# Optimization experiments

Hardware: AMD Instinct MI355X
Metric: run time of the kernel (lower is better)

## Reference

```python
import math
import jax, jax.numpy as jnp
import numpy as np

D_IN = 768      # input_hidden_dim
H = 512         # IDLU_hidden_dim
E = 64          # num_entity
B = 32          # batch_size (mentions)
P = 197         # num_patch (incl. CLS)
RHO = 4.0
EPS = 1e-5


def setup_inputs() -> dict:
    key = jax.random.key(0)
    ks = jax.random.split(key, 16)
    s = 1.0 / math.sqrt(D_IN)
    return {
        "entity_cls": jax.random.normal(ks[0], (E, D_IN), jnp.float32),
        "entity_tokens": jax.random.normal(ks[1], (E, P, D_IN), jnp.float32),
        "mention_image_cls": jax.random.normal(ks[2], (B, D_IN), jnp.float32),
        "mention_image_tokens": jax.random.normal(ks[3], (B, P, D_IN), jnp.float32),
        "mention_patch_mask": jax.random.uniform(ks[4], (B, P), jnp.float32),
        "Wq": jax.random.normal(ks[5], (D_IN, H), jnp.float32) * s,
        "bq": jnp.zeros((H,), jnp.float32),
        "Wk": jax.random.normal(ks[6], (D_IN, H), jnp.float32) * s,
        "bk": jnp.zeros((H,), jnp.float32),
        "Wv": jax.random.normal(ks[7], (D_IN, H), jnp.float32) * s,
        "bv": jnp.zeros((H,), jnp.float32),
        "Wcls": jax.random.normal(ks[8], (D_IN, H), jnp.float32) * s,
        "bcls": jnp.zeros((H,), jnp.float32),
        "ln_g": jnp.ones((H,), jnp.float32),
        "ln_b": jnp.zeros((H,), jnp.float32),
    }


def _layer_norm(x, g, b):
    mu = jnp.mean(x, axis=-1, keepdims=True)
    var = jnp.mean(jnp.square(x - mu), axis=-1, keepdims=True)
    return (x - mu) * jax.lax.rsqrt(var + EPS) * g + b


def reference(entity_cls, entity_tokens, mention_image_cls, mention_image_tokens,
              mention_patch_mask, Wq, bq, Wk, bk, Wv, bv, Wcls, bcls, ln_g, ln_b):
    entity_cls_fc = entity_cls @ Wcls + bcls                      # [E, H]
    q = entity_tokens @ Wq + bq                                   # [E, P, H]
    k = mention_image_tokens @ Wk + bk                            # [B, P, H]
    v = mention_image_tokens @ Wv + bv                            # [B, P, H]
    # broadcast entity x mention attention: [E, B, P, P]
    scores = jnp.einsum('eph,bqh->ebpq', q, k) / math.sqrt(H)
    # additive mask only on the first query row (CLS)
    scores = scores.at[:, :, 0, :].add(RHO * mention_patch_mask[None, :, :])
    probs = jax.nn.softmax(scores, axis=-1)                       # [E, B, P, P]
    context = jnp.einsum('ebpq,bqh->ebph', probs, v)              # [E, B, P, H]
    context = jnp.mean(context, axis=-2)                          # [E, B, H]
    context = _layer_norm(context, ln_g, ln_b)
    g2l = jnp.sum(entity_cls_fc[:, None, :] * context, axis=-1).T # [B, E]
    g2g = mention_image_cls @ entity_cls.T                        # [B, E]
    return (g2l + g2g) / 2
```

## Files before the change

kernel.cpp:

```cpp
#include <hip/hip_runtime.h>
#include <stdint.h>

#define EN 64
#define BN 32
#define PN 197
#define DIN 768
#define HH 512
#define RHO_ 4.0f

typedef __attribute__((ext_vector_type(8))) short bf16x8;
typedef __attribute__((ext_vector_type(4))) float f32x4;

__device__ __forceinline__ ushort f2bf(float f){
  unsigned u = __float_as_uint(f);
  u += 0x7FFFu + ((u >> 16) & 1u);
  return (ushort)(u >> 16);
}
__device__ __forceinline__ float bf2f(ushort h){ return __uint_as_float(((unsigned)h) << 16); }

#define GLOAD_LDS16(g, l) __builtin_amdgcn_global_load_lds( \
    (const __attribute__((address_space(1))) void*)(g), \
    (__attribute__((address_space(3))) void*)(l), 16, 0, 0)

__global__ __launch_bounds__(256) void prep_kernel(
    const float* __restrict__ etok, const float* __restrict__ mtok,
    const float* __restrict__ ecls, const float* __restrict__ bq,
    ushort* __restrict__ a_ent, ushort* __restrict__ a_men, ushort* __restrict__ a_cls,
    float* __restrict__ bq_s)
{
  int g = blockIdx.x*256 + threadIdx.x;
  int st = gridDim.x*256;
  const float s = 0.04419417382415922f;
  for (int i=g; i<(EN*PN*DIN)/4; i+=st){
    float4 v = ((const float4*)etok)[i];
    ushort4 o; o.x=f2bf(v.x); o.y=f2bf(v.y); o.z=f2bf(v.z); o.w=f2bf(v.w);
    ((ushort4*)a_ent)[i] = o;
  }
  for (int i=g; i<(BN*PN*DIN)/4; i+=st){
    float4 v = ((const float4*)mtok)[i];
    ushort4 o; o.x=f2bf(v.x); o.y=f2bf(v.y); o.z=f2bf(v.z); o.w=f2bf(v.w);
    ((ushort4*)a_men)[i] = o;
  }
  for (int i=g; i<(EN*DIN)/4; i+=st){
    float4 v = ((const float4*)ecls)[i];
    ushort4 o; o.x=f2bf(v.x); o.y=f2bf(v.y); o.z=f2bf(v.z); o.w=f2bf(v.w);
    ((ushort4*)a_cls)[i] = o;
  }
  for (int i=g; i<HH; i+=st) bq_s[i] = bq[i]*s;
}

__global__ __launch_bounds__(256) void w_transpose(
    const float* __restrict__ Wq, const float* __restrict__ Wk,
    const float* __restrict__ Wv, const float* __restrict__ Wc,
    ushort* __restrict__ Wt)
{
  __shared__ float tl[64][65];
  int mat = blockIdx.z;
  const float* src = (mat==0)?Wq:(mat==1)?Wk:(mat==2)?Wv:Wc;
  float sc = (mat==0)? 0.04419417382415922f : 1.0f;
  int k0 = blockIdx.x*64;
  int n0 = blockIdx.y*64;
  int tid = threadIdx.x;
  int c = tid & 63, r0 = tid >> 6;
  #pragma unroll
  for (int i=0;i<16;++i){
    int r = r0 + i*4;
    tl[r][c] = src[(size_t)(k0+r)*HH + n0+c];
  }
  __syncthreads();
  ushort* dst = Wt + (size_t)mat*HH*DIN;
  #pragma unroll
  for (int i=0;i<16;++i){
    int r = r0 + i*4;
    dst[(size_t)(n0+r)*DIN + k0+c] = f2bf(tl[c][r]*sc);
  }
}

__global__ __launch_bounds__(256) void gemm_proj(
    const ushort* __restrict__ a_ent, const ushort* __restrict__ a_men, const ushort* __restrict__ a_cls,
    const ushort* __restrict__ Wt,
    const float* __restrict__ bq_s, const float* __restrict__ bk,
    const float* __restrict__ bv, const float* __restrict__ bc,
    ushort* __restrict__ qo, ushort* __restrict__ ko, ushort* __restrict__ vo,
    float* __restrict__ co)
{
  int x = blockIdx.x;
  int op, mt;
  if (x < 99)        { op = 0; mt = x; }
  else if (x < 149)  { op = 1; mt = x - 99; }
  else if (x < 199)  { op = 2; mt = x - 149; }
  else               { op = 3; mt = 0; }
  int M = (op==0)? EN*PN : (op==3)? EN : BN*PN;
  int m0 = mt*128;
  const ushort* A  = (op==0)? a_ent : (op==3)? a_cls : a_men;
  const ushort* Bw = Wt + (size_t)op*HH*DIN;
  const float* bias = (op==0)? bq_s : (op==1)? bk : (op==2)? bv : bc;
  int n0 = blockIdx.y*128;
  int Mm1 = M-1;

  __shared__ ushort As[128*40];
  __shared__ ushort Bs[128*40];
  int tid = threadIdx.x;
  int lane = tid & 63, wid = tid >> 6;
  int l15 = lane & 15, lg = lane >> 4;
  int wm = wid >> 1, wn = wid & 1;

  f32x4 acc[16];
  #pragma unroll
  for (int i=0;i<16;++i){ f32x4 z = {0.f,0.f,0.f,0.f}; acc[i] = z; }

  bf16x8 sA[2], sB[2];
  #pragma unroll
  for (int i=0;i<2;++i){
    int u = tid + i*256; int row = u>>2; int ko8 = (u&3)*8;
    int rA = m0+row; rA = rA>Mm1 ? Mm1 : rA;
    sA[i] = *(const bf16x8*)(A  + (size_t)rA*DIN + ko8);
    sB[i] = *(const bf16x8*)(Bw + (size_t)(n0+row)*DIN + ko8);
  }
  for (int kt=0; kt<DIN/32; ++kt){
    #pragma unroll
    for (int i=0;i<2;++i){
      int u = tid + i*256; int row = u>>2; int ko8 = (u&3)*8;
      *(bf16x8*)(&As[row*40 + ko8]) = sA[i];
      *(bf16x8*)(&Bs[row*40 + ko8]) = sB[i];
    }
    __syncthreads();
    if (kt < DIN/32 - 1){
      int k0 = (kt+1)*32;
      #pragma unroll
      for (int i=0;i<2;++i){
        int u = tid + i*256; int row = u>>2; int ko8 = (u&3)*8;
        int rA = m0+row; rA = rA>Mm1 ? Mm1 : rA;
        sA[i] = *(const bf16x8*)(A  + (size_t)rA*DIN + k0 + ko8);
        sB[i] = *(const bf16x8*)(Bw + (size_t)(n0+row)*DIN + k0 + ko8);
      }
    }
    bf16x8 af[4], bfg[4];
    #pragma unroll
    for (int t=0;t<4;++t){
      af[t]  = *(const bf16x8*)(&As[(wm*64 + t*16 + l15)*40 + lg*8]);
      bfg[t] = *(const bf16x8*)(&Bs[(wn*64 + t*16 + l15)*40 + lg*8]);
    }
    #pragma unroll
    for (int am=0; am<4; ++am)
      #pragma unroll
      for (int bn=0; bn<4; ++bn)
        acc[am*4+bn] = __builtin_amdgcn_mfma_f32_16x16x32_bf16(af[am], bfg[bn], acc[am*4+bn], 0, 0, 0);
    __syncthreads();
  }

  #pragma unroll
  for (int bn=0; bn<4; ++bn){
    int col = n0 + wn*64 + bn*16 + l15;
    float bval = bias[col];
    #pragma unroll
    for (int am=0; am<4; ++am){
      #pragma unroll
      for (int r=0;r<4;++r){
        int row = m0 + wm*64 + am*16 + lg*4 + r;
        if (row < M){
          float v = acc[am*4+bn][r] + bval;
          if (op==3)      co[(size_t)row*HH + col] = v;
          else if (op==0) qo[(size_t)row*HH + col] = f2bf(v);
          else if (op==1) ko[(size_t)row*HH + col] = f2bf(v);
          else            vo[(size_t)row*HH + col] = f2bf(v);
        }
      }
    }
  }
}

__global__ __launch_bounds__(512) void attn_kernel(
    const ushort* __restrict__ qw, const ushort* __restrict__ kw, const ushort* __restrict__ vw,
    const float* __restrict__ cls_fc, const float* __restrict__ maskp,
    const float* __restrict__ mcls, const float* __restrict__ ecls,
    const float* __restrict__ lng, const float* __restrict__ lnb,
    float* __restrict__ outp)
{
  int bid = blockIdx.x;
  int b = bid >> 5;
  int e0 = (bid & 31) * 2;

  __shared__ ushort klds[2][1664*8];
  __shared__ float w_lds[2][208];
  __shared__ float red[32];

  int tid = threadIdx.x;
  int lane = tid & 63, wid = tid >> 6;
  int l15 = lane & 15, lg = (lane >> 4) & 3;

  for (int i=tid; i<416; i+=512) ((float*)w_lds)[i] = 0.f;

  const ushort* kb = kw + (size_t)b*PN*HH;
  const ushort* qb0 = qw + (size_t)e0*PN*HH;
  const ushort* qb1 = qw + (size_t)(e0+1)*PN*HH;

  auto issue = [&](int bf, int kc){
    #pragma unroll
    for (int i=0;i<4;++i){
      int L = tid + i*512;
      if (L < 1664){
        int col = L >> 3, j = L & 7;
        int cg = col > 196 ? 196 : col;
        const ushort* src = kb + (size_t)cg*HH + kc*64 + ((j ^ (col & 7)) * 8);
        ushort* dst = &klds[bf][ (wid*64 + i*512) * 8 ];
        GLOAD_LDS16(src, dst);
      }
    }
  };

  int ar0 = wid*16 + l15;
  int tt1 = 8 + wid;
  int rt1 = tt1 > 12 ? 12 : tt1;
  int ar1 = rt1*16 + l15; ar1 = ar1 > 196 ? 196 : ar1;
  const ushort* q00 = qb0 + (size_t)ar0*HH + lg*8;
  const ushort* q01 = qb1 + (size_t)ar0*HH + lg*8;
  const ushort* q10 = qb0 + (size_t)ar1*HH + lg*8;
  const ushort* q11 = qb1 + (size_t)ar1*HH + lg*8;

  f32x4 acc[2][13];
  #pragma unroll
  for (int e2=0;e2<2;++e2)
    #pragma unroll
    for (int i=0;i<13;++i){ f32x4 z={0.f,0.f,0.f,0.f}; acc[e2][i]=z; }

  issue(0, 0);
  bf16x8 qc[2][2], qn[2][2];
  #pragma unroll
  for (int s=0; s<2; ++s){
    qc[0][s] = *(const bf16x8*)(q00 + s*32);
    qc[1][s] = *(const bf16x8*)(q01 + s*32);
  }

  #pragma unroll 1
  for (int g=0; g<16; ++g){
    int rnd = g >> 3, c = g & 7;
    __syncthreads();
    if (g < 15){
      issue((g+1)&1, (g+1)&7);
      int nkc = (g+1)&7;
      const ushort* a0 = ((g+1)>>3) ? q10 : q00;
      const ushort* a1 = ((g+1)>>3) ? q11 : q01;
      #pragma unroll
      for (int s=0; s<2; ++s){
        qn[0][s] = *(const bf16x8*)(a0 + nkc*64 + s*32);
        qn[1][s] = *(const bf16x8*)(a1 + nkc*64 + s*32);
      }
    }
    int tt = rnd*8 + wid;
    bool active = tt < 13;
    if (active){
      const ushort* kbase = &klds[g&1][0];
      #pragma unroll
      for (int s=0; s<2; ++s){
        int ru = s*4 + lg;
        #pragma unroll
        for (int ct=0; ct<13; ++ct){
          int lcol = ct*16 + l15;
          bf16x8 bfr = *(const bf16x8*)(kbase + (size_t)(lcol*8 + (ru ^ (lcol&7)))*8);
          acc[0][ct] = __builtin_amdgcn_mfma_f32_16x16x32_bf16(qc[0][s], bfr, acc[0][ct], 0,0,0);
          acc[1][ct] = __builtin_amdgcn_mfma_f32_16x16x32_bf16(qc[1][s], bfr, acc[1][ct], 0,0,0);
        }
      }
    }
    #pragma unroll
    for (int s=0; s<2; ++s){ qc[0][s] = qn[0][s]; qc[1][s] = qn[1][s]; }

    if (c == 7){
      if (active){
        int rt = tt > 12 ? 12 : tt;
        #pragma unroll
        for (int e2=0; e2<2; ++e2){
          if (l15 >= 5){
            f32x4 ninf = {-1e30f,-1e30f,-1e30f,-1e30f};
            acc[e2][12] = ninf;
          }
          if (rt==0 && lg==0){
            #pragma unroll
            for (int ct=0; ct<13; ++ct){
              int col = ct*16 + l15;
              if (col < 197) acc[e2][ct][0] += RHO_ * maskp[b*PN + col];
            }
          }
          float mrow[4], inv[4];
          #pragma unroll
          for (int r=0;r<4;++r){
            float m = acc[e2][0][r];
            #pragma unroll
            for (int ct=1; ct<13; ++ct) m = fmaxf(m, acc[e2][ct][r]);
            m = fmaxf(m, __shfl_xor(m,1));
            m = fmaxf(m, __shfl_xor(m,2));
            m = fmaxf(m, __shfl_xor(m,4));
            m = fmaxf(m, __shfl_xor(m,8));
            mrow[r] = m;
          }
          #pragma unroll
          for (int r=0;r<4;++r){
            float sm = 0.f;
            #pragma unroll
            for (int ct=0; ct<13; ++ct){
              float ev = __expf(acc[e2][ct][r] - mrow[r]);
              acc[e2][ct][r] = ev;
              sm += ev;
            }
            sm += __shfl_xor(sm,1); sm += __shfl_xor(sm,2);
            sm += __shfl_xor(sm,4); sm += __shfl_xor(sm,8);
            int prow = rt*16 + lg*4 + r;
            inv[r] = (prow < PN) ? 1.0f/sm : 0.f;
          }
          #pragma unroll
          for (int ct=0; ct<13; ++ct){
            float cs = acc[e2][ct][0]*inv[0] + acc[e2][ct][1]*inv[1]
                     + acc[e2][ct][2]*inv[2] + acc[e2][ct][3]*inv[3];
            cs += __shfl_xor(cs,16);
            cs += __shfl_xor(cs,32);
            if (lg==0) atomicAdd(&w_lds[e2][ct*16 + l15], cs);
          }
        }
      }
      if (rnd == 0){
        #pragma unroll
        for (int e2=0;e2<2;++e2)
          #pragma unroll
          for (int i=0;i<13;++i){ f32x4 z={0.f,0.f,0.f,0.f}; acc[e2][i]=z; }
      }
    }
  }
  __syncthreads();

  const ushort* vb = vw + (size_t)b*PN*HH;
  float cA=0.f, cB=0.f;
  #pragma unroll 4
  for (int q=0; q<PN; ++q){
    float vq = bf2f(vb[(size_t)q*HH + tid]);
    cA += w_lds[0][q]*vq;
    cB += w_lds[1][q]*vq;
  }
  const float invP = 1.0f/197.0f;
  cA*=invP; cB*=invP;

  float sx = cA, sxx = cA*cA, sy = cB, syy = cB*cB;
  #pragma unroll
  for (int off=32; off; off>>=1){
    sx += __shfl_down(sx, off); sxx += __shfl_down(sxx, off);
    sy += __shfl_down(sy, off); syy += __shfl_down(syy, off);
  }
  if (lane==0){ red[wid*4+0]=sx; red[wid*4+1]=sxx; red[wid*4+2]=sy; red[wid*4+3]=syy; }
  __syncthreads();
  float s1A=0.f, s2A=0.f, s1B=0.f, s2B=0.f;
  #pragma unroll
  for (int w=0; w<8; ++w){
    s1A += red[w*4+0]; s2A += red[w*4+1];
    s1B += red[w*4+2]; s2B += red[w*4+3];
  }
  float muA = s1A*(1.f/512.f), muB = s1B*(1.f/512.f);
  float varA = s2A*(1.f/512.f) - muA*muA;
  float varB = s2B*(1.f/512.f) - muB*muB;
  float rsA = rsqrtf(varA + 1e-5f), rsB = rsqrtf(varB + 1e-5f);

  int h = tid;
  float g0=lng[h], bb0=lnb[h];
  float dA = ((cA-muA)*rsA*g0 + bb0) * cls_fc[(size_t)e0*HH + h];
  float dB = ((cB-muB)*rsB*g0 + bb0) * cls_fc[(size_t)(e0+1)*HH + h];

  dA += mcls[b*DIN + tid]*ecls[(size_t)e0*DIN + tid];
  dB += mcls[b*DIN + tid]*ecls[(size_t)(e0+1)*DIN + tid];
  if (tid < 256){
    int j = tid + 512;
    dA += mcls[b*DIN + j]*ecls[(size_t)e0*DIN + j];
    dB += mcls[b*DIN + j]*ecls[(size_t)(e0+1)*DIN + j];
  }

  __syncthreads();
  #pragma unroll
  for (int off=32; off; off>>=1){ dA += __shfl_down(dA, off); dB += __shfl_down(dB, off); }
  if (lane==0){ red[wid*2+0]=dA; red[wid*2+1]=dB; }
  __syncthreads();
  if (tid==0){
    float oA=0.f, oB=0.f;
    #pragma unroll
    for (int w=0; w<8; ++w){ oA += red[w*2+0]; oB += red[w*2+1]; }
    outp[b*EN + e0]   = 0.5f*oA;
    outp[b*EN + e0+1] = 0.5f*oB;
  }
}

extern "C" void kernel_launch(void* const* d_in, const int* in_sizes, int n_in,
                              void* d_out, int out_size, void* d_ws, size_t ws_size,
                              hipStream_t stream)
{
  (void)in_sizes; (void)n_in; (void)out_size; (void)ws_size;
  const float* ecls = (const float*)d_in[0];
  const float* etok = (const float*)d_in[1];
  const float* mcls = (const float*)d_in[2];
  const float* mtok = (const float*)d_in[3];
  const float* maskp= (const float*)d_in[4];
  const float* Wq   = (const float*)d_in[5];
  const float* bq   = (const float*)d_in[6];
  const float* Wk   = (const float*)d_in[7];
  const float* bk   = (const float*)d_in[8];
  const float* Wv   = (const float*)d_in[9];
  const float* bv   = (const float*)d_in[10];
  const float* Wc   = (const float*)d_in[11];
  const float* bc   = (const float*)d_in[12];
  const float* lng  = (const float*)d_in[13];
  const float* lnb  = (const float*)d_in[14];

  char* ws = (char*)d_ws;
  size_t off = 0;
  auto take = [&](size_t bytes){ char* p = ws + off; off += (bytes + 255) & ~(size_t)255; return p; };
  ushort* a_ent = (ushort*)take((size_t)EN*PN*DIN*2);
  ushort* a_men = (ushort*)take((size_t)BN*PN*DIN*2);
  ushort* a_cls = (ushort*)take((size_t)EN*DIN*2);
  ushort* Wt    = (ushort*)take((size_t)4*HH*DIN*2);
  float*  bq_s  = (float*)take((size_t)HH*4);
  ushort* qo    = (ushort*)take((size_t)EN*PN*HH*2);
  ushort* ko    = (ushort*)take((size_t)BN*PN*HH*2);
  ushort* vo    = (ushort*)take((size_t)BN*PN*HH*2);
  float*  co    = (float*)take((size_t)EN*HH*4);

  prep_kernel<<<1024, 256, 0, stream>>>(etok, mtok, ecls, bq, a_ent, a_men, a_cls, bq_s);
  w_transpose<<<dim3(12,8,4), 256, 0, stream>>>(Wq, Wk, Wv, Wc, Wt);
  gemm_proj<<<dim3(200,4,1), 256, 0, stream>>>(a_ent, a_men, a_cls, Wt,
                                               bq_s, bk, bv, bc, qo, ko, vo, co);
  attn_kernel<<<1024, 512, 0, stream>>>(qo, ko, vo, co, maskp, mcls, ecls,
                                        lng, lnb, (float*)d_out);
}
```

Before: 472.9 us.

## Shrink attention block to four waves with four row-tile passes

The attention kernel now runs with 256 threads (4 waves) instead of 512. Each wave covers the 13 query row tiles over four passes of the 8 K chunks rather than two, and each thread handles two hidden columns in the V/LayerNorm epilogue. MFMA sections are wrapped in s_setprio to raise wave priority during matrix math. The aim is less idle-wave waste (the old 8-wave layout left 3 waves inactive in the second round) and possibly higher occupancy per CU. The cost is twice as many K chunk reloads and barriers per block.

```diff
diff --git a/kernel.cpp b/kernel.cpp
--- a/kernel.cpp
+++ b/kernel.cpp
@@ -170,7 +170,7 @@
   }
 }
 
-__global__ __launch_bounds__(512) void attn_kernel(
+__global__ __launch_bounds__(256) void attn_kernel(
     const ushort* __restrict__ qw, const ushort* __restrict__ kw, const ushort* __restrict__ vw,
     const float* __restrict__ cls_fc, const float* __restrict__ maskp,
     const float* __restrict__ mcls, const float* __restrict__ ecls,
@@ -183,41 +183,32 @@
 
   __shared__ ushort klds[2][1664*8];
   __shared__ float w_lds[2][208];
-  __shared__ float red[32];
+  __shared__ float red[16];
 
   int tid = threadIdx.x;
   int lane = tid & 63, wid = tid >> 6;
   int l15 = lane & 15, lg = (lane >> 4) & 3;
 
-  for (int i=tid; i<416; i+=512) ((float*)w_lds)[i] = 0.f;
-
-  const ushort* kb = kw + (size_t)b*PN*HH;
+  for (int i=tid; i<416; i+=256) ((float*)w_lds)[i] = 0.f;
+
+  const ushort* kb  = kw + (size_t)b*PN*HH;
   const ushort* qb0 = qw + (size_t)e0*PN*HH;
   const ushort* qb1 = qw + (size_t)(e0+1)*PN*HH;
 
   auto issue = [&](int bf, int kc){
     #pragma unroll
-    for (int i=0;i<4;++i){
-      int L = tid + i*512;
+    for (int i=0;i<7;++i){
+      int L = tid + i*256;
       if (L < 1664){
         int col = L >> 3, j = L & 7;
         int cg = col > 196 ? 196 : col;
         const ushort* src = kb + (size_t)cg*HH + kc*64 + ((j ^ (col & 7)) * 8);
-        ushort* dst = &klds[bf][ (wid*64 + i*512) * 8 ];
+        ushort* dst = &klds[bf][ (wid*64 + i*256) * 8 ];
         GLOAD_LDS16(src, dst);
       }
     }
   };
 
-  int ar0 = wid*16 + l15;
-  int tt1 = 8 + wid;
-  int rt1 = tt1 > 12 ? 12 : tt1;
-  int ar1 = rt1*16 + l15; ar1 = ar1 > 196 ? 196 : ar1;
-  const ushort* q00 = qb0 + (size_t)ar0*HH + lg*8;
-  const ushort* q01 = qb1 + (size_t)ar0*HH + lg*8;
-  const ushort* q10 = qb0 + (size_t)ar1*HH + lg*8;
-  const ushort* q11 = qb1 + (size_t)ar1*HH + lg*8;
-
   f32x4 acc[2][13];
   #pragma unroll
   for (int e2=0;e2<2;++e2)
@@ -225,32 +216,35 @@
     for (int i=0;i<13;++i){ f32x4 z={0.f,0.f,0.f,0.f}; acc[e2][i]=z; }
 
   issue(0, 0);
-  bf16x8 qc[2][2], qn[2][2];
-  #pragma unroll
-  for (int s=0; s<2; ++s){
-    qc[0][s] = *(const bf16x8*)(q00 + s*32);
-    qc[1][s] = *(const bf16x8*)(q01 + s*32);
+  bf16x8 qc[2][2];
+  {
+    int r0 = wid*16 + l15;
+    const ushort* a0 = qb0 + (size_t)r0*HH + lg*8;
+    const ushort* a1 = qb1 + (size_t)r0*HH + lg*8;
+    qc[0][0] = *(const bf16x8*)a0; qc[0][1] = *(const bf16x8*)(a0+32);
+    qc[1][0] = *(const bf16x8*)a1; qc[1][1] = *(const bf16x8*)(a1+32);
   }
 
   #pragma unroll 1
-  for (int g=0; g<16; ++g){
-    int rnd = g >> 3, c = g & 7;
+  for (int g=0; g<32; ++g){
+    int pass = g >> 3, kc = g & 7;
+    int slot = pass*4 + wid;
+    bool active = slot < 13;
     __syncthreads();
-    if (g < 15){
-      issue((g+1)&1, (g+1)&7);
-      int nkc = (g+1)&7;
-      const ushort* a0 = ((g+1)>>3) ? q10 : q00;
-      const ushort* a1 = ((g+1)>>3) ? q11 : q01;
-      #pragma unroll
-      for (int s=0; s<2; ++s){
-        qn[0][s] = *(const bf16x8*)(a0 + nkc*64 + s*32);
-        qn[1][s] = *(const bf16x8*)(a1 + nkc*64 + s*32);
-      }
-    }
-    int tt = rnd*8 + wid;
-    bool active = tt < 13;
+    if (g < 31) issue((g+1)&1, (g+1)&7);
+    bf16x8 qn[2][2];
+    if (g < 31){
+      int np = (g+1)>>3, nkc = (g+1)&7;
+      int ns = np*4 + wid; ns = ns > 12 ? 12 : ns;
+      int nr = ns*16 + l15; nr = nr > 196 ? 196 : nr;
+      const ushort* a0 = qb0 + (size_t)nr*HH + nkc*64 + lg*8;
+      const ushort* a1 = qb1 + (size_t)nr*HH + nkc*64 + lg*8;
+      qn[0][0] = *(const bf16x8*)a0; qn[0][1] = *(const bf16x8*)(a0+32);
+      qn[1][0] = *(const bf16x8*)a1; qn[1][1] = *(const bf16x8*)(a1+32);
+    }
     if (active){
       const ushort* kbase = &klds[g&1][0];
+      __builtin_amdgcn_s_setprio(1);
       #pragma unroll
       for (int s=0; s<2; ++s){
         int ru = s*4 + lg;
@@ -262,13 +256,14 @@
           acc[1][ct] = __builtin_amdgcn_mfma_f32_16x16x32_bf16(qc[1][s], bfr, acc[1][ct], 0,0,0);
         }
       }
-    }
-    #pragma unroll
-    for (int s=0; s<2; ++s){ qc[0][s] = qn[0][s]; qc[1][s] = qn[1][s]; }
-
-    if (c == 7){
+      __builtin_amdgcn_s_setprio(0);
+    }
+    #pragma unroll
+    for (int s=0; s<2; ++s){ qc[0][s]=qn[0][s]; qc[1][s]=qn[1][s]; }
+
+    if (kc == 7){
       if (active){
-        int rt = tt > 12 ? 12 : tt;
+        int rt = slot;
         #pragma unroll
         for (int e2=0; e2<2; ++e2){
           if (l15 >= 5){
@@ -318,7 +313,7 @@
           }
         }
       }
-      if (rnd == 0){
+      if (pass < 3){
         #pragma unroll
         for (int e2=0;e2<2;++e2)
           #pragma unroll
@@ -329,17 +324,20 @@
   __syncthreads();
 
   const ushort* vb = vw + (size_t)b*PN*HH;
-  float cA=0.f, cB=0.f;
+  float cA0=0.f, cA1=0.f, cB0=0.f, cB1=0.f;
   #pragma unroll 4
   for (int q=0; q<PN; ++q){
-    float vq = bf2f(vb[(size_t)q*HH + tid]);
-    cA += w_lds[0][q]*vq;
-    cB += w_lds[1][q]*vq;
+    float v0 = bf2f(vb[(size_t)q*HH + tid]);
+    float v1 = bf2f(vb[(size_t)q*HH + tid + 256]);
+    float w0 = w_lds[0][q], w1 = w_lds[1][q];
+    cA0 += w0*v0; cA1 += w0*v1;
+    cB0 += w1*v0; cB1 += w1*v1;
   }
   const float invP = 1.0f/197.0f;
-  cA*=invP; cB*=invP;
-
-  float sx = cA, sxx = cA*cA, sy = cB, syy = cB*cB;
+  cA0*=invP; cA1*=invP; cB0*=invP; cB1*=invP;
+
+  float sx = cA0+cA1, sxx = cA0*cA0+cA1*cA1;
+  float sy = cB0+cB1, syy = cB0*cB0+cB1*cB1;
   #pragma unroll
   for (int off=32; off; off>>=1){
     sx += __shfl_down(sx, off); sxx += __shfl_down(sxx, off);
@@ -347,29 +345,26 @@
   }
   if (lane==0){ red[wid*4+0]=sx; red[wid*4+1]=sxx; red[wid*4+2]=sy; red[wid*4+3]=syy; }
   __syncthreads();
-  float s1A=0.f, s2A=0.f, s1B=0.f, s2B=0.f;
-  #pragma unroll
-  for (int w=0; w<8; ++w){
-    s1A += red[w*4+0]; s2A += red[w*4+1];
-    s1B += red[w*4+2]; s2B += red[w*4+3];
-  }
+  float s1A = red[0]+red[4]+red[8]+red[12];
+  float s2A = red[1]+red[5]+red[9]+red[13];
+  float s1B = red[2]+red[6]+red[10]+red[14];
+  float s2B = red[3]+red[7]+red[11]+red[15];
   float muA = s1A*(1.f/512.f), muB = s1B*(1.f/512.f);
   float varA = s2A*(1.f/512.f) - muA*muA;
   float varB = s2B*(1.f/512.f) - muB*muB;
   float rsA = rsqrtf(varA + 1e-5f), rsB = rsqrtf(varB + 1e-5f);
 
-  int h = tid;
-  float g0=lng[h], bb0=lnb[h];
-  float dA = ((cA-muA)*rsA*g0 + bb0) * cls_fc[(size_t)e0*HH + h];
-  float dB = ((cB-muB)*rsB*g0 + bb0) * cls_fc[(size_t)(e0+1)*HH + h];
-
-  dA += mcls[b*DIN + tid]*ecls[(size_t)e0*DIN + tid];
-  dB += mcls[b*DIN + tid]*ecls[(size_t)(e0+1)*DIN + tid];
-  if (tid < 256){
-    int j = tid + 512;
-    dA += mcls[b*DIN + j]*ecls[(size_t)e0*DIN + j];
-    dB += mcls[b*DIN + j]*ecls[(size_t)(e0+1)*DIN + j];
-  }
+  int h0 = tid, h1 = tid + 256;
+  float g0=lng[h0], g1=lng[h1], bb0=lnb[h0], bb1=lnb[h1];
+  float fA0 = cls_fc[(size_t)e0*HH + h0],     fA1 = cls_fc[(size_t)e0*HH + h1];
+  float fB0 = cls_fc[(size_t)(e0+1)*HH + h0], fB1 = cls_fc[(size_t)(e0+1)*HH + h1];
+  float dA = ((cA0-muA)*rsA*g0 + bb0)*fA0 + ((cA1-muA)*rsA*g1 + bb1)*fA1;
+  float dB = ((cB0-muB)*rsB*g0 + bb0)*fB0 + ((cB1-muB)*rsB*g1 + bb1)*fB1;
+
+  int j = 3*tid;
+  float m0v = mcls[b*DIN + j], m1v = mcls[b*DIN + j+1], m2v = mcls[b*DIN + j+2];
+  dA += m0v*ecls[(size_t)e0*DIN + j] + m1v*ecls[(size_t)e0*DIN + j+1] + m2v*ecls[(size_t)e0*DIN + j+2];
+  dB += m0v*ecls[(size_t)(e0+1)*DIN + j] + m1v*ecls[(size_t)(e0+1)*DIN + j+1] + m2v*ecls[(size_t)(e0+1)*DIN + j+2];
 
   __syncthreads();
   #pragma unroll
@@ -377,11 +372,8 @@
   if (lane==0){ red[wid*2+0]=dA; red[wid*2+1]=dB; }
   __syncthreads();
   if (tid==0){
-    float oA=0.f, oB=0.f;
-    #pragma unroll
-    for (int w=0; w<8; ++w){ oA += red[w*2+0]; oB += red[w*2+1]; }
-    outp[b*EN + e0]   = 0.5f*oA;
-    outp[b*EN + e0+1] = 0.5f*oB;
+    outp[b*EN + e0]   = 0.5f*(red[0]+red[2]+red[4]+red[6]);
+    outp[b*EN + e0+1] = 0.5f*(red[1]+red[3]+red[5]+red[7]);
   }
 }
 
@@ -423,6 +415,6 @@
   w_transpose<<<dim3(12,8,4), 256, 0, stream>>>(Wq, Wk, Wv, Wc, Wt);
   gemm_proj<<<dim3(200,4,1), 256, 0, stream>>>(a_ent, a_men, a_cls, Wt,
                                                bq_s, bk, bv, bc, qo, ko, vo, co);
-  attn_kernel<<<1024, 512, 0, stream>>>(qo, ko, vo, co, maskp, mcls, ecls,
+  attn_kernel<<<1024, 256, 0, stream>>>(qo, ko, vo, co, maskp, mcls, ecls,
                                         lng, lnb, (float*)d_out);
 }
```

Result: slower. 602.2 us (+27.3%).

## Load K fragments directly from global memory instead of staging through LDS

Applied to the files above, without the earlier changes.

Removes the double-buffered LDS staging of K (global_load_lds plus a __syncthreads per step) from the attention scores loop. Each wave now reads its own 13 K fragments straight from global memory per k-step and processes its row tiles in two independent rounds. This is meant to cut block-wide barriers and LDS traffic, at the cost of every wave re-reading the whole K tile from L2. The global reads are also poorly coalesced, with only 64 contiguous bytes per row, and register pressure rises. The padded columns 197..207 are no longer clamped, so they read beyond the batch's K rows (and past the buffer end for the last batch), though those scores are masked out afterwards.

```diff
diff --git a/kernel.cpp b/kernel.cpp
--- a/kernel.cpp
+++ b/kernel.cpp
@@ -17,10 +17,6 @@
   return (ushort)(u >> 16);
 }
 __device__ __forceinline__ float bf2f(ushort h){ return __uint_as_float(((unsigned)h) << 16); }
-
-#define GLOAD_LDS16(g, l) __builtin_amdgcn_global_load_lds( \
-    (const __attribute__((address_space(1))) void*)(g), \
-    (__attribute__((address_space(3))) void*)(l), 16, 0, 0)
 
 __global__ __launch_bounds__(256) void prep_kernel(
     const float* __restrict__ etok, const float* __restrict__ mtok,
@@ -181,7 +177,6 @@
   int b = bid >> 5;
   int e0 = (bid & 31) * 2;
 
-  __shared__ ushort klds[2][1664*8];
   __shared__ float w_lds[2][208];
   __shared__ float red[32];
 
@@ -190,139 +185,93 @@
   int l15 = lane & 15, lg = (lane >> 4) & 3;
 
   for (int i=tid; i<416; i+=512) ((float*)w_lds)[i] = 0.f;
-
-  const ushort* kb = kw + (size_t)b*PN*HH;
+  __syncthreads();
+
+  const ushort* kb  = kw + (size_t)b*PN*HH;
   const ushort* qb0 = qw + (size_t)e0*PN*HH;
   const ushort* qb1 = qw + (size_t)(e0+1)*PN*HH;
 
-  auto issue = [&](int bf, int kc){
-    #pragma unroll
-    for (int i=0;i<4;++i){
-      int L = tid + i*512;
-      if (L < 1664){
-        int col = L >> 3, j = L & 7;
-        int cg = col > 196 ? 196 : col;
-        const ushort* src = kb + (size_t)cg*HH + kc*64 + ((j ^ (col & 7)) * 8);
-        ushort* dst = &klds[bf][ (wid*64 + i*512) * 8 ];
-        GLOAD_LDS16(src, dst);
+  int voff[13];
+  #pragma unroll
+  for (int ct=0; ct<13; ++ct) voff[ct] = (ct*16 + l15)*HH + lg*8;
+
+  for (int rnd=0; rnd<2; ++rnd){
+    int slot = rnd*8 + wid;
+    bool active = slot < 13;
+    if (active){
+      int arow = slot*16 + l15; arow = arow > 196 ? 196 : arow;
+      const ushort* q0 = qb0 + (size_t)arow*HH + lg*8;
+      const ushort* q1 = qb1 + (size_t)arow*HH + lg*8;
+
+      f32x4 acc[2][13];
+      #pragma unroll
+      for (int e2=0;e2<2;++e2)
+        #pragma unroll
+        for (int i=0;i<13;++i){ f32x4 z={0.f,0.f,0.f,0.f}; acc[e2][i]=z; }
+
+      #pragma unroll
+      for (int s=0; s<16; ++s){
+        bf16x8 bfr[13];
+        #pragma unroll
+        for (int ct=0; ct<13; ++ct)
+          bfr[ct] = *(const bf16x8*)(kb + voff[ct] + s*32);
+        bf16x8 qa = *(const bf16x8*)(q0 + s*32);
+        bf16x8 qc = *(const bf16x8*)(q1 + s*32);
+        #pragma unroll
+        for (int ct=0; ct<13; ++ct){
+          acc[0][ct] = __builtin_amdgcn_mfma_f32_16x16x32_bf16(qa, bfr[ct], acc[0][ct], 0,0,0);
+          acc[1][ct] = __builtin_amdgcn_mfma_f32_16x16x32_bf16(qc, bfr[ct], acc[1][ct], 0,0,0);
+        }
       }
-    }
-  };
-
-  int ar0 = wid*16 + l15;
-  int tt1 = 8 + wid;
-  int rt1 = tt1 > 12 ? 12 : tt1;
-  int ar1 = rt1*16 + l15; ar1 = ar1 > 196 ? 196 : ar1;
-  const ushort* q00 = qb0 + (size_t)ar0*HH + lg*8;
-  const ushort* q01 = qb1 + (size_t)ar0*HH + lg*8;
-  const ushort* q10 = qb0 + (size_t)ar1*HH + lg*8;
-  const ushort* q11 = qb1 + (size_t)ar1*HH + lg*8;
-
-  f32x4 acc[2][13];
-  #pragma unroll
-  for (int e2=0;e2<2;++e2)
-    #pragma unroll
-    for (int i=0;i<13;++i){ f32x4 z={0.f,0.f,0.f,0.f}; acc[e2][i]=z; }
-
-  issue(0, 0);
-  bf16x8 qc[2][2], qn[2][2];
-  #pragma unroll
-  for (int s=0; s<2; ++s){
-    qc[0][s] = *(const bf16x8*)(q00 + s*32);
-    qc[1][s] = *(const bf16x8*)(q01 + s*32);
-  }
-
-  #pragma unroll 1
-  for (int g=0; g<16; ++g){
-    int rnd = g >> 3, c = g & 7;
-    __syncthreads();
-    if (g < 15){
-      issue((g+1)&1, (g+1)&7);
-      int nkc = (g+1)&7;
-      const ushort* a0 = ((g+1)>>3) ? q10 : q00;
-      const ushort* a1 = ((g+1)>>3) ? q11 : q01;
-      #pragma unroll
-      for (int s=0; s<2; ++s){
-        qn[0][s] = *(const bf16x8*)(a0 + nkc*64 + s*32);
-        qn[1][s] = *(const bf16x8*)(a1 + nkc*64 + s*32);
-      }
-    }
-    int tt = rnd*8 + wid;
-    bool active = tt < 13;
-    if (active){
-      const ushort* kbase = &klds[g&1][0];
-      #pragma unroll
-      for (int s=0; s<2; ++s){
-        int ru = s*4 + lg;
-        #pragma unroll
-        for (int ct=0; ct<13; ++ct){
-          int lcol = ct*16 + l15;
-          bf16x8 bfr = *(const bf16x8*)(kbase + (size_t)(lcol*8 + (ru ^ (lcol&7)))*8);
-          acc[0][ct] = __builtin_amdgcn_mfma_f32_16x16x32_bf16(qc[0][s], bfr, acc[0][ct], 0,0,0);
-          acc[1][ct] = __builtin_amdgcn_mfma_f32_16x16x32_bf16(qc[1][s], bfr, acc[1][ct], 0,0,0);
-        }
-      }
-    }
-    #pragma unroll
-    for (int s=0; s<2; ++s){ qc[0][s] = qn[0][s]; qc[1][s] = qn[1][s]; }
-
-    if (c == 7){
-      if (active){
-        int rt = tt > 12 ? 12 : tt;
-        #pragma unroll
-        for (int e2=0; e2<2; ++e2){
-          if (l15 >= 5){
-            f32x4 ninf = {-1e30f,-1e30f,-1e30f,-1e30f};
-            acc[e2][12] = ninf;
-          }
-          if (rt==0 && lg==0){
-            #pragma unroll
-            for (int ct=0; ct<13; ++ct){
-              int col = ct*16 + l15;
-              if (col < 197) acc[e2][ct][0] += RHO_ * maskp[b*PN + col];
-            }
-          }
-          float mrow[4], inv[4];
-          #pragma unroll
-          for (int r=0;r<4;++r){
-            float m = acc[e2][0][r];
-            #pragma unroll
-            for (int ct=1; ct<13; ++ct) m = fmaxf(m, acc[e2][ct][r]);
-            m = fmaxf(m, __shfl_xor(m,1));
-            m = fmaxf(m, __shfl_xor(m,2));
-            m = fmaxf(m, __shfl_xor(m,4));
-            m = fmaxf(m, __shfl_xor(m,8));
-            mrow[r] = m;
-          }
-          #pragma unroll
-          for (int r=0;r<4;++r){
-            float sm = 0.f;
-            #pragma unroll
-            for (int ct=0; ct<13; ++ct){
-              float ev = __expf(acc[e2][ct][r] - mrow[r]);
-              acc[e2][ct][r] = ev;
-              sm += ev;
-            }
-            sm += __shfl_xor(sm,1); sm += __shfl_xor(sm,2);
-            sm += __shfl_xor(sm,4); sm += __shfl_xor(sm,8);
-            int prow = rt*16 + lg*4 + r;
-            inv[r] = (prow < PN) ? 1.0f/sm : 0.f;
-          }
+
+      int rt = slot;
+      #pragma unroll
+      for (int e2=0; e2<2; ++e2){
+        if (l15 >= 5){
+          f32x4 ninf = {-1e30f,-1e30f,-1e30f,-1e30f};
+          acc[e2][12] = ninf;
+        }
+        if (rt==0 && lg==0){
           #pragma unroll
           for (int ct=0; ct<13; ++ct){
-            float cs = acc[e2][ct][0]*inv[0] + acc[e2][ct][1]*inv[1]
-                     + acc[e2][ct][2]*inv[2] + acc[e2][ct][3]*inv[3];
-            cs += __shfl_xor(cs,16);
-            cs += __shfl_xor(cs,32);
-            if (lg==0) atomicAdd(&w_lds[e2][ct*16 + l15], cs);
+            int col = ct*16 + l15;
+            if (col < 197) acc[e2][ct][0] += RHO_ * maskp[b*PN + col];
           }
         }
-      }
-      if (rnd == 0){
-        #pragma unroll
-        for (int e2=0;e2<2;++e2)
+        float mrow[4], inv[4];
+        #pragma unroll
+        for (int r=0;r<4;++r){
+          float m = acc[e2][0][r];
           #pragma unroll
-          for (int i=0;i<13;++i){ f32x4 z={0.f,0.f,0.f,0.f}; acc[e2][i]=z; }
+          for (int ct=1; ct<13; ++ct) m = fmaxf(m, acc[e2][ct][r]);
+          m = fmaxf(m, __shfl_xor(m,1));
+          m = fmaxf(m, __shfl_xor(m,2));
+          m = fmaxf(m, __shfl_xor(m,4));
+          m = fmaxf(m, __shfl_xor(m,8));
+          mrow[r] = m;
+        }
+        #pragma unroll
+        for (int r=0;r<4;++r){
+          float sm = 0.f;
+          #pragma unroll
+          for (int ct=0; ct<13; ++ct){
+            float ev = __expf(acc[e2][ct][r] - mrow[r]);
+            acc[e2][ct][r] = ev;
+            sm += ev;
+          }
+          sm += __shfl_xor(sm,1); sm += __shfl_xor(sm,2);
+          sm += __shfl_xor(sm,4); sm += __shfl_xor(sm,8);
+          int prow = rt*16 + lg*4 + r;
+          inv[r] = (prow < PN) ? 1.0f/sm : 0.f;
+        }
+        #pragma unroll
+        for (int ct=0; ct<13; ++ct){
+          float cs = acc[e2][ct][0]*inv[0] + acc[e2][ct][1]*inv[1]
+                   + acc[e2][ct][2]*inv[2] + acc[e2][ct][3]*inv[3];
+          cs += __shfl_xor(cs,16);
+          cs += __shfl_xor(cs,32);
+          if (lg==0) atomicAdd(&w_lds[e2][ct*16 + l15], cs);
+        }
       }
     }
   }
```

Result: slower. 1.153 ms (+143.9%).
